# Kernel optimization log

Hardware: AMD Instinct MI355X
Metric: run time of the kernel (lower is better)

The kernel has to match this reference:

```python
import jax, jax.numpy as jnp
import numpy as np

B, S, H = 16, 4096, 512

def setup_inputs() -> dict:
    key = jax.random.key(0)
    k1, k2, k3, k4, k5 = jax.random.split(key, 5)
    hidden = jax.random.normal(k1, (B, H), dtype=jnp.float32)
    encoder_outputs = jax.random.normal(k2, (B, S, 2 * H), dtype=jnp.float32)
    # nn.Linear(3H, H): weight [H, 3H], bias [H]
    W_attn = jax.random.normal(k3, (H, 3 * H), dtype=jnp.float32) * (1.0 / np.sqrt(3 * H))
    b_attn = jax.random.normal(k4, (H,), dtype=jnp.float32) * 0.01
    v = jax.random.normal(k5, (H,), dtype=jnp.float32)
    return {"hidden": hidden, "encoder_outputs": encoder_outputs,
            "W_attn": W_attn, "b_attn": b_attn, "v": v}

def reference(hidden, encoder_outputs, W_attn, b_attn, v):
    src_len = encoder_outputs.shape[1]
    # [B, S, H] broadcast of decoder hidden, concat with encoder outputs -> [B, S, 3H]
    h_rep = jnp.broadcast_to(hidden[:, None, :], (hidden.shape[0], src_len, hidden.shape[1]))
    combined = jnp.concatenate([h_rep, encoder_outputs], axis=2)
    energy = jnp.tanh(jnp.einsum('bsf,hf->bsh', combined, W_attn) + b_attn)
    attention = jnp.einsum('bsh,h->bs', energy, v)  # bmm(v, energy.T) squeezed
    return jax.nn.softmax(attention, axis=1)
```

## Files before the change

### kernel.cpp

```cpp
#include <hip/hip_runtime.h>

typedef __attribute__((ext_vector_type(4))) float f32x4;
typedef __attribute__((ext_vector_type(8))) short bf16x8;
typedef __attribute__((ext_vector_type(4))) short bf16x4;

#define MEMBAR() asm volatile("" ::: "memory")

__device__ __forceinline__ unsigned short f2bf(float f) {
  unsigned int u = __builtin_bit_cast(unsigned int, f);
  u += 0x7FFFu + ((u >> 16) & 1u);
  return (unsigned short)(u >> 16);
}

__global__ __launch_bounds__(256) void k_prep_p(
    const float* __restrict__ hidden, const float* __restrict__ W,
    const float* __restrict__ bias, float* __restrict__ P) {
  __shared__ float hsh[512];
  const int b = blockIdx.x;
  for (int i = threadIdx.x; i < 512; i += 256) hsh[i] = hidden[b * 512 + i];
  __syncthreads();
  for (int h = threadIdx.x; h < 512; h += 256) {
    const float* wr = W + (long)h * 1536;
    float s = 0.f;
#pragma unroll 4
    for (int f = 0; f < 512; f += 4) {
      float4 wv = *reinterpret_cast<const float4*>(wr + f);
      s += wv.x * hsh[f] + wv.y * hsh[f + 1] + wv.z * hsh[f + 2] + wv.w * hsh[f + 3];
    }
    P[b * 512 + h] = bias[h] + s;
  }
}

__global__ __launch_bounds__(256) void k_prep_w(
    const float* __restrict__ W, unsigned short* __restrict__ W2t) {
  const int id = blockIdx.x * 256 + threadIdx.x;
  const int kk8 = (id & 3) * 8;
  const int h = (id >> 2) & 511;
  const int kb = id >> 11;
  const float* src = W + (long)h * 1536 + 512 + kb * 32 + kk8;
  float4 a = *reinterpret_cast<const float4*>(src);
  float4 c = *reinterpret_cast<const float4*>(src + 4);
  union { unsigned short u[8]; bf16x8 v; } o;
  o.u[0] = f2bf(a.x); o.u[1] = f2bf(a.y); o.u[2] = f2bf(a.z); o.u[3] = f2bf(a.w);
  o.u[4] = f2bf(c.x); o.u[5] = f2bf(c.y); o.u[6] = f2bf(c.z); o.u[7] = f2bf(c.w);
  *reinterpret_cast<bf16x8*>(W2t + (long)kb * 16384 + h * 32 + kk8) = o.v;
}

__global__ __launch_bounds__(512, 2) void k_main(
    const float* __restrict__ enc, const short* __restrict__ W2t,
    const float* __restrict__ P, const float* __restrict__ v,
    float* __restrict__ logits) {
  __shared__ short As[4][2048];
  __shared__ float attred[64][8];

  const int tid = threadIdx.x;
  const int lane = tid & 63;
  const int w = tid >> 6;
  const int hl = lane & 15, kg = lane >> 4;
  const long rowbase = (long)blockIdx.x * 64;
  const int b = (int)(rowbase >> 12);

  const int r = tid >> 3, c = tid & 7;
  const f32x4* gp = reinterpret_cast<const f32x4*>(enc + (rowbase + r) * 1024) + c;
  const int wr_off = r * 32 + ((((c >> 1) ^ ((r >> 1) & 3)) << 3)) + ((c & 1) << 2);
  const int base_f = hl * 32 + ((kg ^ ((hl >> 1) & 3)) << 3);
  const short* bp = W2t + (w * 64 + hl) * 32 + kg * 8;

  f32x4 acc[4][4];
#pragma unroll
  for (int mi = 0; mi < 4; ++mi)
#pragma unroll
    for (int ni = 0; ni < 4; ++ni) acc[mi][ni] = (f32x4){0.f, 0.f, 0.f, 0.f};

  bf16x8 Ba[4], Bb[4];
  f32x4 rawE, rawO;

#define CVT4W(BUF, RAW) {                                             \
    union { __bf16 h[4]; bf16x4 s; } _u;                              \
    _u.h[0] = (__bf16)(RAW)[0]; _u.h[1] = (__bf16)(RAW)[1];           \
    _u.h[2] = (__bf16)(RAW)[2]; _u.h[3] = (__bf16)(RAW)[3];           \
    *reinterpret_cast<bf16x4*>(&As[(BUF)][wr_off]) = _u.s;            \
  }
#define LOADB(DST, KB) {                                              \
    const short* _k = bp + (KB) * 16384;                              \
    DST[0] = *reinterpret_cast<const bf16x8*>(_k);                    \
    DST[1] = *reinterpret_cast<const bf16x8*>(_k + 512);              \
    DST[2] = *reinterpret_cast<const bf16x8*>(_k + 1024);             \
    DST[3] = *reinterpret_cast<const bf16x8*>(_k + 1536);             \
  }
#define K_ITER(J, RAWIN, RAWOUT, BIN, BOUT, DO_G, DO_B, DO_CVT) {     \
    MEMBAR();                                                         \
    __builtin_amdgcn_s_barrier();                                     \
    MEMBAR();                                                         \
    if (DO_G) RAWOUT = gp[((J) + 2) * 8];                             \
    if (DO_B) LOADB(BOUT, (J) + 1);                                   \
    MEMBAR();                                                         \
    const short* _ab = &As[(J) & 3][0];                               \
    bf16x8 _f0 = *reinterpret_cast<const bf16x8*>(_ab + base_f);      \
    bf16x8 _f1 = *reinterpret_cast<const bf16x8*>(_ab + base_f + 512);\
    bf16x8 _f2 = *reinterpret_cast<const bf16x8*>(_ab + base_f + 1024);\
    bf16x8 _f3 = *reinterpret_cast<const bf16x8*>(_ab + base_f + 1536);\
    acc[0][0] = __builtin_amdgcn_mfma_f32_16x16x32_bf16(_f0, BIN[0], acc[0][0], 0, 0, 0); \
    acc[0][1] = __builtin_amdgcn_mfma_f32_16x16x32_bf16(_f0, BIN[1], acc[0][1], 0, 0, 0); \
    acc[0][2] = __builtin_amdgcn_mfma_f32_16x16x32_bf16(_f0, BIN[2], acc[0][2], 0, 0, 0); \
    acc[0][3] = __builtin_amdgcn_mfma_f32_16x16x32_bf16(_f0, BIN[3], acc[0][3], 0, 0, 0); \
    acc[1][0] = __builtin_amdgcn_mfma_f32_16x16x32_bf16(_f1, BIN[0], acc[1][0], 0, 0, 0); \
    acc[1][1] = __builtin_amdgcn_mfma_f32_16x16x32_bf16(_f1, BIN[1], acc[1][1], 0, 0, 0); \
    acc[1][2] = __builtin_amdgcn_mfma_f32_16x16x32_bf16(_f1, BIN[2], acc[1][2], 0, 0, 0); \
    acc[1][3] = __builtin_amdgcn_mfma_f32_16x16x32_bf16(_f1, BIN[3], acc[1][3], 0, 0, 0); \
    acc[2][0] = __builtin_amdgcn_mfma_f32_16x16x32_bf16(_f2, BIN[0], acc[2][0], 0, 0, 0); \
    acc[2][1] = __builtin_amdgcn_mfma_f32_16x16x32_bf16(_f2, BIN[1], acc[2][1], 0, 0, 0); \
    acc[2][2] = __builtin_amdgcn_mfma_f32_16x16x32_bf16(_f2, BIN[2], acc[2][2], 0, 0, 0); \
    acc[2][3] = __builtin_amdgcn_mfma_f32_16x16x32_bf16(_f2, BIN[3], acc[2][3], 0, 0, 0); \
    acc[3][0] = __builtin_amdgcn_mfma_f32_16x16x32_bf16(_f3, BIN[0], acc[3][0], 0, 0, 0); \
    acc[3][1] = __builtin_amdgcn_mfma_f32_16x16x32_bf16(_f3, BIN[1], acc[3][1], 0, 0, 0); \
    acc[3][2] = __builtin_amdgcn_mfma_f32_16x16x32_bf16(_f3, BIN[2], acc[3][2], 0, 0, 0); \
    acc[3][3] = __builtin_amdgcn_mfma_f32_16x16x32_bf16(_f3, BIN[3], acc[3][3], 0, 0, 0); \
    if (DO_CVT) CVT4W(((J) + 1) & 3, RAWIN);                          \
    asm volatile("s_waitcnt lgkmcnt(0)" ::: "memory");                \
  }

  {
    f32x4 raw0 = gp[0];
    CVT4W(0, raw0);
  }
  rawO = gp[8];
  LOADB(Ba, 0);
  __syncthreads();

#pragma unroll 1
  for (int p = 0; p < 15; ++p) {
    const int j = p * 2;
    K_ITER(j,     rawO, rawE, Ba, Bb, 1, 1, 1);
    K_ITER(j + 1, rawE, rawO, Bb, Ba, 1, 1, 1);
  }
  K_ITER(30, rawO, rawE, Ba, Bb, 0, 1, 1);
  K_ITER(31, rawE, rawO, Bb, Ba, 0, 0, 0);

#undef K_ITER
#undef LOADB
#undef CVT4W

  float part[4][4];
#pragma unroll
  for (int mi = 0; mi < 4; ++mi)
#pragma unroll
    for (int rr = 0; rr < 4; ++rr) part[mi][rr] = 0.f;

#pragma unroll
  for (int ni = 0; ni < 4; ++ni) {
    const int h = w * 64 + ni * 16 + hl;
    const float ph = P[b * 512 + h];
    const float vh = v[h];
#pragma unroll
    for (int mi = 0; mi < 4; ++mi)
#pragma unroll
      for (int rr = 0; rr < 4; ++rr) {
        float x = acc[mi][ni][rr] + ph;
        float e = __expf(2.f * x);
        part[mi][rr] += vh * (1.f - 2.f * __frcp_rn(e + 1.f));
      }
  }
#pragma unroll
  for (int off = 1; off < 16; off <<= 1)
#pragma unroll
    for (int mi = 0; mi < 4; ++mi)
#pragma unroll
      for (int rr = 0; rr < 4; ++rr)
        part[mi][rr] += __shfl_xor(part[mi][rr], off, 16);

  if (hl == 0) {
#pragma unroll
    for (int mi = 0; mi < 4; ++mi)
#pragma unroll
      for (int rr = 0; rr < 4; ++rr)
        attred[mi * 16 + kg * 4 + rr][w] = part[mi][rr];
  }
  __syncthreads();
  if (tid < 64) {
    const float* a = attred[tid];
    logits[rowbase + tid] = ((a[0] + a[1]) + (a[2] + a[3])) +
                            ((a[4] + a[5]) + (a[6] + a[7]));
  }
}

__global__ __launch_bounds__(256) void k_softmax(
    const float* __restrict__ logits, float* __restrict__ out) {
  const int b = blockIdx.x;
  const int t = threadIdx.x;
  const int wid = t >> 6, lane = t & 63;
  const float* L = logits + b * 4096;
  __shared__ float rmax[4], rsum[4];
  float lv[16];
  float m = -1e30f;
#pragma unroll
  for (int i = 0; i < 16; ++i) {
    lv[i] = L[t + i * 256];
    m = fmaxf(m, lv[i]);
  }
#pragma unroll
  for (int off = 32; off >= 1; off >>= 1) m = fmaxf(m, __shfl_xor(m, off));
  if (lane == 0) rmax[wid] = m;
  __syncthreads();
  m = fmaxf(fmaxf(rmax[0], rmax[1]), fmaxf(rmax[2], rmax[3]));
  float s = 0.f;
#pragma unroll
  for (int i = 0; i < 16; ++i) {
    lv[i] = __expf(lv[i] - m);
    s += lv[i];
  }
#pragma unroll
  for (int off = 32; off >= 1; off >>= 1) s += __shfl_xor(s, off);
  if (lane == 0) rsum[wid] = s;
  __syncthreads();
  s = rsum[0] + rsum[1] + rsum[2] + rsum[3];
  float inv = 1.0f / s;
#pragma unroll
  for (int i = 0; i < 16; ++i) out[b * 4096 + t + i * 256] = lv[i] * inv;
}

extern "C" void kernel_launch(void* const* d_in, const int* in_sizes, int n_in,
                              void* d_out, int out_size, void* d_ws, size_t ws_size,
                              hipStream_t stream) {
  const float* hidden = (const float*)d_in[0];
  const float* enc    = (const float*)d_in[1];
  const float* W      = (const float*)d_in[2];
  const float* bias   = (const float*)d_in[3];
  const float* v      = (const float*)d_in[4];
  float* out = (float*)d_out;

  char* ws = (char*)d_ws;
  float* P = (float*)ws;
  unsigned short* W2t = (unsigned short*)(ws + 32768);
  float* logits = (float*)(ws + 32768 + 1048576);

  k_prep_p<<<16, 256, 0, stream>>>(hidden, W, bias, P);
  k_prep_w<<<256, 256, 0, stream>>>(W, W2t);
  k_main<<<1024, 512, 0, stream>>>(enc, (const short*)W2t, P, v, logits);
  k_softmax<<<16, 256, 0, stream>>>(logits, out);
}
```

Measured before the change: 138.7 us.

## Process two K-chunks per barrier in main GEMM loop

Restructures the main k-loop so each barrier-separated step consumes two 32-wide K slices: two global f32 loads and two LDS conversions per step, with the 4-slot LDS ring reorganised as two ping-pong pairs. The B-operand register buffers are split into even and odd sets, and the even set's next load is issued between the two MFMA groups. This halves the number of workgroup barriers and waitcnt drains per K range, aiming to cut sync overhead and give loads more time to overlap. The prefetch distance is now one double-step rather than two single steps, which may expose more global latency, and the extra raw registers add register pressure.

```diff
diff --git a/kernel.cpp b/kernel.cpp
--- a/kernel.cpp
+++ b/kernel.cpp
@@ -61,7 +61,7 @@
   const int b = (int)(rowbase >> 12);
 
   const int r = tid >> 3, c = tid & 7;
-  const f32x4* gp = reinterpret_cast<const f32x4*>(enc + (rowbase + r) * 1024) + c;
+  const f32x4* gp = reinterpret_cast<const f32x4*>(enc + (rowbase + r) * 1024);
   const int wr_off = r * 32 + ((((c >> 1) ^ ((r >> 1) & 3)) << 3)) + ((c & 1) << 2);
   const int base_f = hl * 32 + ((kg ^ ((hl >> 1) & 3)) << 3);
   const short* bp = W2t + (w * 64 + hl) * 32 + kg * 8;
@@ -72,8 +72,8 @@
 #pragma unroll
     for (int ni = 0; ni < 4; ++ni) acc[mi][ni] = (f32x4){0.f, 0.f, 0.f, 0.f};
 
-  bf16x8 Ba[4], Bb[4];
-  f32x4 rawE, rawO;
+  bf16x8 Se[4], So[4];
+  f32x4 rawA, rawB;
 
 #define CVT4W(BUF, RAW) {                                             \
     union { __bf16 h[4]; bf16x4 s; } _u;                              \
@@ -88,56 +88,66 @@
     DST[2] = *reinterpret_cast<const bf16x8*>(_k + 1024);             \
     DST[3] = *reinterpret_cast<const bf16x8*>(_k + 1536);             \
   }
-#define K_ITER(J, RAWIN, RAWOUT, BIN, BOUT, DO_G, DO_B, DO_CVT) {     \
+#define MFMA16(AB, BS) {                                              \
+    bf16x8 _f0 = *reinterpret_cast<const bf16x8*>((AB) + base_f);     \
+    bf16x8 _f1 = *reinterpret_cast<const bf16x8*>((AB) + base_f + 512); \
+    bf16x8 _f2 = *reinterpret_cast<const bf16x8*>((AB) + base_f + 1024); \
+    bf16x8 _f3 = *reinterpret_cast<const bf16x8*>((AB) + base_f + 1536); \
+    acc[0][0] = __builtin_amdgcn_mfma_f32_16x16x32_bf16(_f0, BS[0], acc[0][0], 0, 0, 0); \
+    acc[0][1] = __builtin_amdgcn_mfma_f32_16x16x32_bf16(_f0, BS[1], acc[0][1], 0, 0, 0); \
+    acc[0][2] = __builtin_amdgcn_mfma_f32_16x16x32_bf16(_f0, BS[2], acc[0][2], 0, 0, 0); \
+    acc[0][3] = __builtin_amdgcn_mfma_f32_16x16x32_bf16(_f0, BS[3], acc[0][3], 0, 0, 0); \
+    acc[1][0] = __builtin_amdgcn_mfma_f32_16x16x32_bf16(_f1, BS[0], acc[1][0], 0, 0, 0); \
+    acc[1][1] = __builtin_amdgcn_mfma_f32_16x16x32_bf16(_f1, BS[1], acc[1][1], 0, 0, 0); \
+    acc[1][2] = __builtin_amdgcn_mfma_f32_16x16x32_bf16(_f1, BS[2], acc[1][2], 0, 0, 0); \
+    acc[1][3] = __builtin_amdgcn_mfma_f32_16x16x32_bf16(_f1, BS[3], acc[1][3], 0, 0, 0); \
+    acc[2][0] = __builtin_amdgcn_mfma_f32_16x16x32_bf16(_f2, BS[0], acc[2][0], 0, 0, 0); \
+    acc[2][1] = __builtin_amdgcn_mfma_f32_16x16x32_bf16(_f2, BS[1], acc[2][1], 0, 0, 0); \
+    acc[2][2] = __builtin_amdgcn_mfma_f32_16x16x32_bf16(_f2, BS[2], acc[2][2], 0, 0, 0); \
+    acc[2][3] = __builtin_amdgcn_mfma_f32_16x16x32_bf16(_f2, BS[3], acc[2][3], 0, 0, 0); \
+    acc[3][0] = __builtin_amdgcn_mfma_f32_16x16x32_bf16(_f3, BS[0], acc[3][0], 0, 0, 0); \
+    acc[3][1] = __builtin_amdgcn_mfma_f32_16x16x32_bf16(_f3, BS[1], acc[3][1], 0, 0, 0); \
+    acc[3][2] = __builtin_amdgcn_mfma_f32_16x16x32_bf16(_f3, BS[2], acc[3][2], 0, 0, 0); \
+    acc[3][3] = __builtin_amdgcn_mfma_f32_16x16x32_bf16(_f3, BS[3], acc[3][3], 0, 0, 0); \
+  }
+#define K_ITER(J, PP, DO_G, DO_SE) {                                  \
     MEMBAR();                                                         \
     __builtin_amdgcn_s_barrier();                                     \
     MEMBAR();                                                         \
-    if (DO_G) RAWOUT = gp[((J) + 2) * 8];                             \
-    if (DO_B) LOADB(BOUT, (J) + 1);                                   \
+    if (DO_G) {                                                       \
+      rawA = gp[((J) + 1) * 16 + c];                                  \
+      rawB = gp[((J) + 1) * 16 + 8 + c];                              \
+    }                                                                 \
+    LOADB(So, 2 * (J) + 1);                                           \
     MEMBAR();                                                         \
-    const short* _ab = &As[(J) & 3][0];                               \
-    bf16x8 _f0 = *reinterpret_cast<const bf16x8*>(_ab + base_f);      \
-    bf16x8 _f1 = *reinterpret_cast<const bf16x8*>(_ab + base_f + 512);\
-    bf16x8 _f2 = *reinterpret_cast<const bf16x8*>(_ab + base_f + 1024);\
-    bf16x8 _f3 = *reinterpret_cast<const bf16x8*>(_ab + base_f + 1536);\
-    acc[0][0] = __builtin_amdgcn_mfma_f32_16x16x32_bf16(_f0, BIN[0], acc[0][0], 0, 0, 0); \
-    acc[0][1] = __builtin_amdgcn_mfma_f32_16x16x32_bf16(_f0, BIN[1], acc[0][1], 0, 0, 0); \
-    acc[0][2] = __builtin_amdgcn_mfma_f32_16x16x32_bf16(_f0, BIN[2], acc[0][2], 0, 0, 0); \
-    acc[0][3] = __builtin_amdgcn_mfma_f32_16x16x32_bf16(_f0, BIN[3], acc[0][3], 0, 0, 0); \
-    acc[1][0] = __builtin_amdgcn_mfma_f32_16x16x32_bf16(_f1, BIN[0], acc[1][0], 0, 0, 0); \
-    acc[1][1] = __builtin_amdgcn_mfma_f32_16x16x32_bf16(_f1, BIN[1], acc[1][1], 0, 0, 0); \
-    acc[1][2] = __builtin_amdgcn_mfma_f32_16x16x32_bf16(_f1, BIN[2], acc[1][2], 0, 0, 0); \
-    acc[1][3] = __builtin_amdgcn_mfma_f32_16x16x32_bf16(_f1, BIN[3], acc[1][3], 0, 0, 0); \
-    acc[2][0] = __builtin_amdgcn_mfma_f32_16x16x32_bf16(_f2, BIN[0], acc[2][0], 0, 0, 0); \
-    acc[2][1] = __builtin_amdgcn_mfma_f32_16x16x32_bf16(_f2, BIN[1], acc[2][1], 0, 0, 0); \
-    acc[2][2] = __builtin_amdgcn_mfma_f32_16x16x32_bf16(_f2, BIN[2], acc[2][2], 0, 0, 0); \
-    acc[2][3] = __builtin_amdgcn_mfma_f32_16x16x32_bf16(_f2, BIN[3], acc[2][3], 0, 0, 0); \
-    acc[3][0] = __builtin_amdgcn_mfma_f32_16x16x32_bf16(_f3, BIN[0], acc[3][0], 0, 0, 0); \
-    acc[3][1] = __builtin_amdgcn_mfma_f32_16x16x32_bf16(_f3, BIN[1], acc[3][1], 0, 0, 0); \
-    acc[3][2] = __builtin_amdgcn_mfma_f32_16x16x32_bf16(_f3, BIN[2], acc[3][2], 0, 0, 0); \
-    acc[3][3] = __builtin_amdgcn_mfma_f32_16x16x32_bf16(_f3, BIN[3], acc[3][3], 0, 0, 0); \
-    if (DO_CVT) CVT4W(((J) + 1) & 3, RAWIN);                          \
+    MFMA16(&As[2 * (PP)][0], Se)                                      \
+    if (DO_SE) LOADB(Se, 2 * (J) + 2);                                \
+    MFMA16(&As[2 * (PP) + 1][0], So)                                  \
+    if (DO_G) {                                                       \
+      CVT4W(2 * (1 - (PP)), rawA);                                    \
+      CVT4W(2 * (1 - (PP)) + 1, rawB);                                \
+    }                                                                 \
     asm volatile("s_waitcnt lgkmcnt(0)" ::: "memory");                \
   }
 
-  {
-    f32x4 raw0 = gp[0];
-    CVT4W(0, raw0);
-  }
-  rawO = gp[8];
-  LOADB(Ba, 0);
-  __syncthreads();
+  rawA = gp[c];
+  rawB = gp[8 + c];
+  CVT4W(0, rawA);
+  CVT4W(1, rawB);
+  LOADB(Se, 0);
+  asm volatile("s_waitcnt lgkmcnt(0)" ::: "memory");
 
 #pragma unroll 1
-  for (int p = 0; p < 15; ++p) {
+  for (int p = 0; p < 7; ++p) {
     const int j = p * 2;
-    K_ITER(j,     rawO, rawE, Ba, Bb, 1, 1, 1);
-    K_ITER(j + 1, rawE, rawO, Bb, Ba, 1, 1, 1);
-  }
-  K_ITER(30, rawO, rawE, Ba, Bb, 0, 1, 1);
-  K_ITER(31, rawE, rawO, Bb, Ba, 0, 0, 0);
+    K_ITER(j,     0, 1, 1)
+    K_ITER(j + 1, 1, 1, 1)
+  }
+  K_ITER(14, 0, 1, 1)
+  K_ITER(15, 1, 0, 0)
 
 #undef K_ITER
+#undef MFMA16
 #undef LOADB
 #undef CVT4W
 
```

Result: slower. 160.0 us (+15.4%).

## Halve main-kernel row tile to 32 rows and double occupancy

Applied to the files above, without the earlier changes.

Shrinks the per-block M tile from 64 to 32 encoder rows, doubling the grid to 2048 blocks. Each thread now loads two floats per k-step instead of four, with a new LDS swizzle, and launch bounds allow 4 blocks per CU. The aim is more blocks in flight and lower register pressure to hide memory latency. The cost is that every block still streams all of W2t, so weight traffic per output row doubles and MFMA work per barrier halves.

```diff
diff --git a/kernel.cpp b/kernel.cpp
--- a/kernel.cpp
+++ b/kernel.cpp
@@ -1,8 +1,8 @@
 #include <hip/hip_runtime.h>
 
 typedef __attribute__((ext_vector_type(4))) float f32x4;
+typedef __attribute__((ext_vector_type(2))) float f32x2;
 typedef __attribute__((ext_vector_type(8))) short bf16x8;
-typedef __attribute__((ext_vector_type(4))) short bf16x4;
 
 #define MEMBAR() asm volatile("" ::: "memory")
 
@@ -46,40 +46,39 @@
   *reinterpret_cast<bf16x8*>(W2t + (long)kb * 16384 + h * 32 + kk8) = o.v;
 }
 
-__global__ __launch_bounds__(512, 2) void k_main(
+__global__ __launch_bounds__(512, 4) void k_main(
     const float* __restrict__ enc, const short* __restrict__ W2t,
     const float* __restrict__ P, const float* __restrict__ v,
     float* __restrict__ logits) {
-  __shared__ short As[4][2048];
-  __shared__ float attred[64][8];
+  __shared__ short As[4][1024];
+  __shared__ float attred[32][8];
 
   const int tid = threadIdx.x;
   const int lane = tid & 63;
   const int w = tid >> 6;
   const int hl = lane & 15, kg = lane >> 4;
-  const long rowbase = (long)blockIdx.x * 64;
+  const long rowbase = (long)blockIdx.x * 32;
   const int b = (int)(rowbase >> 12);
 
-  const int r = tid >> 3, c = tid & 7;
-  const f32x4* gp = reinterpret_cast<const f32x4*>(enc + (rowbase + r) * 1024) + c;
-  const int wr_off = r * 32 + ((((c >> 1) ^ ((r >> 1) & 3)) << 3)) + ((c & 1) << 2);
-  const int base_f = hl * 32 + ((kg ^ ((hl >> 1) & 3)) << 3);
+  const int r = tid >> 4, c = tid & 15;
+  const float* ga = enc + (rowbase + r) * 1024 + c * 2;
+  const int wr_off = r * 32 + (((c >> 2) ^ (r & 3)) << 3) + ((c & 3) << 1);
+  const int base_f = hl * 32 + ((kg ^ (hl & 3)) << 3);
   const short* bp = W2t + (w * 64 + hl) * 32 + kg * 8;
 
-  f32x4 acc[4][4];
-#pragma unroll
-  for (int mi = 0; mi < 4; ++mi)
+  f32x4 acc[2][4];
+#pragma unroll
+  for (int mi = 0; mi < 2; ++mi)
 #pragma unroll
     for (int ni = 0; ni < 4; ++ni) acc[mi][ni] = (f32x4){0.f, 0.f, 0.f, 0.f};
 
   bf16x8 Ba[4], Bb[4];
-  f32x4 rawE, rawO;
-
-#define CVT4W(BUF, RAW) {                                             \
-    union { __bf16 h[4]; bf16x4 s; } _u;                              \
-    _u.h[0] = (__bf16)(RAW)[0]; _u.h[1] = (__bf16)(RAW)[1];           \
-    _u.h[2] = (__bf16)(RAW)[2]; _u.h[3] = (__bf16)(RAW)[3];           \
-    *reinterpret_cast<bf16x4*>(&As[(BUF)][wr_off]) = _u.s;            \
+  f32x2 rawE, rawO;
+
+#define CVT2W(BUF, RAW) {                                             \
+    union { unsigned short u[2]; unsigned int d; } _u;                \
+    _u.u[0] = f2bf((RAW)[0]); _u.u[1] = f2bf((RAW)[1]);               \
+    *reinterpret_cast<unsigned int*>(&As[(BUF)][wr_off]) = _u.d;      \
   }
 #define LOADB(DST, KB) {                                              \
     const short* _k = bp + (KB) * 16384;                              \
@@ -92,14 +91,12 @@
     MEMBAR();                                                         \
     __builtin_amdgcn_s_barrier();                                     \
     MEMBAR();                                                         \
-    if (DO_G) RAWOUT = gp[((J) + 2) * 8];                             \
+    if (DO_G) RAWOUT = *reinterpret_cast<const f32x2*>(ga + ((J) + 2) * 32); \
     if (DO_B) LOADB(BOUT, (J) + 1);                                   \
     MEMBAR();                                                         \
     const short* _ab = &As[(J) & 3][0];                               \
     bf16x8 _f0 = *reinterpret_cast<const bf16x8*>(_ab + base_f);      \
     bf16x8 _f1 = *reinterpret_cast<const bf16x8*>(_ab + base_f + 512);\
-    bf16x8 _f2 = *reinterpret_cast<const bf16x8*>(_ab + base_f + 1024);\
-    bf16x8 _f3 = *reinterpret_cast<const bf16x8*>(_ab + base_f + 1536);\
     acc[0][0] = __builtin_amdgcn_mfma_f32_16x16x32_bf16(_f0, BIN[0], acc[0][0], 0, 0, 0); \
     acc[0][1] = __builtin_amdgcn_mfma_f32_16x16x32_bf16(_f0, BIN[1], acc[0][1], 0, 0, 0); \
     acc[0][2] = __builtin_amdgcn_mfma_f32_16x16x32_bf16(_f0, BIN[2], acc[0][2], 0, 0, 0); \
@@ -108,42 +105,34 @@
     acc[1][1] = __builtin_amdgcn_mfma_f32_16x16x32_bf16(_f1, BIN[1], acc[1][1], 0, 0, 0); \
     acc[1][2] = __builtin_amdgcn_mfma_f32_16x16x32_bf16(_f1, BIN[2], acc[1][2], 0, 0, 0); \
     acc[1][3] = __builtin_amdgcn_mfma_f32_16x16x32_bf16(_f1, BIN[3], acc[1][3], 0, 0, 0); \
-    acc[2][0] = __builtin_amdgcn_mfma_f32_16x16x32_bf16(_f2, BIN[0], acc[2][0], 0, 0, 0); \
-    acc[2][1] = __builtin_amdgcn_mfma_f32_16x16x32_bf16(_f2, BIN[1], acc[2][1], 0, 0, 0); \
-    acc[2][2] = __builtin_amdgcn_mfma_f32_16x16x32_bf16(_f2, BIN[2], acc[2][2], 0, 0, 0); \
-    acc[2][3] = __builtin_amdgcn_mfma_f32_16x16x32_bf16(_f2, BIN[3], acc[2][3], 0, 0, 0); \
-    acc[3][0] = __builtin_amdgcn_mfma_f32_16x16x32_bf16(_f3, BIN[0], acc[3][0], 0, 0, 0); \
-    acc[3][1] = __builtin_amdgcn_mfma_f32_16x16x32_bf16(_f3, BIN[1], acc[3][1], 0, 0, 0); \
-    acc[3][2] = __builtin_amdgcn_mfma_f32_16x16x32_bf16(_f3, BIN[2], acc[3][2], 0, 0, 0); \
-    acc[3][3] = __builtin_amdgcn_mfma_f32_16x16x32_bf16(_f3, BIN[3], acc[3][3], 0, 0, 0); \
-    if (DO_CVT) CVT4W(((J) + 1) & 3, RAWIN);                          \
+    if (DO_CVT) CVT2W(((J) + 1) & 3, RAWIN);                          \
     asm volatile("s_waitcnt lgkmcnt(0)" ::: "memory");                \
   }
 
   {
-    f32x4 raw0 = gp[0];
-    CVT4W(0, raw0);
-  }
-  rawO = gp[8];
+    f32x2 t0 = *reinterpret_cast<const f32x2*>(ga);
+    CVT2W(0, t0);
+  }
+  rawO = *reinterpret_cast<const f32x2*>(ga + 32);
   LOADB(Ba, 0);
   __syncthreads();
 
 #pragma unroll 1
   for (int p = 0; p < 15; ++p) {
     const int j = p * 2;
-    K_ITER(j,     rawO, rawE, Ba, Bb, 1, 1, 1);
-    K_ITER(j + 1, rawE, rawO, Bb, Ba, 1, 1, 1);
-  }
-  K_ITER(30, rawO, rawE, Ba, Bb, 0, 1, 1);
-  K_ITER(31, rawE, rawO, Bb, Ba, 0, 0, 0);
+    K_ITER(j,     rawO, rawE, Ba, Bb, 1, 1, 1)
+    K_ITER(j + 1, rawE, rawO, Bb, Ba, 1, 1, 1)
+  }
+  K_ITER(30, rawO, rawE, Ba, Bb, 0, 1, 1)
+  K_ITER(31, rawE, rawO, Bb, Ba, 0, 0, 0)
 
 #undef K_ITER
 #undef LOADB
-#undef CVT4W
-
-  float part[4][4];
-#pragma unroll
-  for (int mi = 0; mi < 4; ++mi)
+#undef CVT2W
+
+  float part[2][4];
+#pragma unroll
+  for (int mi = 0; mi < 2; ++mi)
 #pragma unroll
     for (int rr = 0; rr < 4; ++rr) part[mi][rr] = 0.f;
 
@@ -153,7 +142,7 @@
     const float ph = P[b * 512 + h];
     const float vh = v[h];
 #pragma unroll
-    for (int mi = 0; mi < 4; ++mi)
+    for (int mi = 0; mi < 2; ++mi)
 #pragma unroll
       for (int rr = 0; rr < 4; ++rr) {
         float x = acc[mi][ni][rr] + ph;
@@ -164,20 +153,20 @@
 #pragma unroll
   for (int off = 1; off < 16; off <<= 1)
 #pragma unroll
-    for (int mi = 0; mi < 4; ++mi)
+    for (int mi = 0; mi < 2; ++mi)
 #pragma unroll
       for (int rr = 0; rr < 4; ++rr)
         part[mi][rr] += __shfl_xor(part[mi][rr], off, 16);
 
   if (hl == 0) {
 #pragma unroll
-    for (int mi = 0; mi < 4; ++mi)
+    for (int mi = 0; mi < 2; ++mi)
 #pragma unroll
       for (int rr = 0; rr < 4; ++rr)
         attred[mi * 16 + kg * 4 + rr][w] = part[mi][rr];
   }
   __syncthreads();
-  if (tid < 64) {
+  if (tid < 32) {
     const float* a = attred[tid];
     logits[rowbase + tid] = ((a[0] + a[1]) + (a[2] + a[3])) +
                             ((a[4] + a[5]) + (a[6] + a[7]));
@@ -236,6 +225,6 @@
 
   k_prep_p<<<16, 256, 0, stream>>>(hidden, W, bias, P);
   k_prep_w<<<256, 256, 0, stream>>>(W, W2t);
-  k_main<<<1024, 512, 0, stream>>>(enc, (const short*)W2t, P, v, logits);
+  k_main<<<2048, 512, 0, stream>>>(enc, (const short*)W2t, P, v, logits);
   k_softmax<<<16, 256, 0, stream>>>(logits, out);
 }
```

Result: slower. 184.7 us (+33.2%).
